# Optimization experiments

Hardware: AMD Instinct MI355X
Metric: run time of the kernel (lower is better)

The kernel has to match this reference:

```python
import jax, jax.numpy as jnp
import numpy as np

STRIDE = 1
PAD = 1


def setup_inputs() -> dict:
    key = jax.random.key(0)
    k1, k2, k3 = jax.random.split(key, 3)
    # Single image (C_in, H, W) as in the original unbatched HETensor list layout
    x = jax.random.normal(k1, (256, 512, 512), dtype=jnp.float32)
    # Weights in HWIO layout (kh, kw, C_in, C_out) matching load_weights' expected shape
    W = jax.random.normal(k2, (3, 3, 256, 256), dtype=jnp.float32) * 0.02
    b = jax.random.normal(k3, (256,), dtype=jnp.float32)
    return {"x": x, "W": W, "b": b}


def reference(x, W, b):
    # Zero-pad then convolve; out_h = ceil((H + 2*PAD - kh + 1)/STRIDE) == lax conv output for stride 1
    out = jax.lax.conv_general_dilated(
        x[None],                      # [1, C_in, H, W]
        W,                            # [kh, kw, C_in, C_out]
        window_strides=(STRIDE, STRIDE),
        padding=[(PAD, PAD), (PAD, PAD)],
        dimension_numbers=("NCHW", "HWIO", "NCHW"),
    )
    return out[0] + b[:, None, None]  # [C_out, H, W]
```

## Files before the change

kernel.cpp:

```cpp
#include <hip/hip_runtime.h>
#include <hip/hip_bf16.h>


typedef __attribute__((ext_vector_type(8))) short bf16x8;
typedef __attribute__((ext_vector_type(4))) float floatx4;

#define HWSZ 262144
#define CIN  256
#define HH   512
#define WWD  512

__device__ __forceinline__ void async_copy16(const void* g, void* l) {
  __builtin_amdgcn_global_load_lds(
      (const __attribute__((address_space(1))) void*)g,
      (__attribute__((address_space(3))) void*)l, 16, 0, 0);
}

__global__ __launch_bounds__(256) void convert_x(
    const float* __restrict__ x, __hip_bfloat16* __restrict__ xt)
{
  __shared__ __align__(16) unsigned char lds[64 * 512];
  const int b  = blockIdx.x;
  const int wt = b & 7;
  const int h  = b >> 3;
  const int w0 = wt << 6;
  const int t  = threadIdx.x;

  const int lane16 = t & 15;
  const int cidx   = t >> 4;
  const float* xrow = x + (size_t)h * WWD + w0 + lane16 * 4;
#pragma unroll 4
  for (int cit = 0; cit < 16; ++cit) {
    int ci = cit * 16 + cidx;
    float4 v = *(const float4*)(xrow + (size_t)ci * HWSZ);
    float f[4] = {v.x, v.y, v.z, v.w};
#pragma unroll
    for (int j = 0; j < 4; ++j) {
      int p = lane16 * 4 + j;
      int chunk = (ci >> 3) ^ (p >> 2);
      *(__hip_bfloat16*)&lds[p * 512 + chunk * 16 + (ci & 7) * 2] =
          __float2bfloat16(f[j]);
    }
  }
  __syncthreads();

  const int m  = t & 31;
  const int pq = t >> 5;
#pragma unroll
  for (int it = 0; it < 8; ++it) {
    int p = it * 8 + pq;
    uint4 v = *(const uint4*)&lds[p * 512 + ((m ^ (p >> 2)) << 4)];
    *(uint4*)&xt[(((size_t)h * WWD + w0 + p) << 8) + m * 8] = v;
  }
}

__global__ __launch_bounds__(256) void convert_w(
    const float* __restrict__ Wf, __hip_bfloat16* __restrict__ wt,
    __hip_bfloat16* __restrict__ zb)
{
  const int idx = blockIdx.x * 256 + threadIdx.x;
  const int ci = idx & 255;
  const int co = (idx >> 8) & 255;
  const int kk = idx >> 16;
  wt[((size_t)(kk * 256 + co) << 8) + ci] =
      __float2bfloat16(Wf[((size_t)(kk * 256 + ci) << 8) + co]);
  if (idx < 64) zb[idx] = __float2bfloat16(0.0f);
}

__global__ __launch_bounds__(256, 3) void conv_mfma(
    const __hip_bfloat16* __restrict__ xt,
    const __hip_bfloat16* __restrict__ wt,
    const float* __restrict__ bias,
    float* __restrict__ out,
    const __hip_bfloat16* __restrict__ zb)
{
  __shared__ __align__(16) __hip_bfloat16 As[3 * 128 * 32];
  __shared__ __align__(16) __hip_bfloat16 Bs[130 * 32];

  const int b    = blockIdx.x;
  const int wti  = b & 3;
  const int cot  = (b >> 2) & 1;
  const int h    = b >> 3;
  const int w0   = wti << 7;
  const int co0  = cot << 7;
  const int t    = threadIdx.x;
  const int lane = t & 63;
  const int wave = t >> 6;
  const int wm   = wave & 1;
  const int wn   = wave >> 1;
  const int mcol = lane & 15;
  const int krow = lane >> 4;

  floatx4 acc[4][4];
#pragma unroll
  for (int mi = 0; mi < 4; ++mi)
#pragma unroll
    for (int ni = 0; ni < 4; ++ni) {
      floatx4 z = {0.f, 0.f, 0.f, 0.f};
      acc[mi][ni] = z;
    }

  for (int kh = 0; kh < 3; ++kh) {
    const int hp = h + kh - 1;
    const bool hok = (unsigned)hp < (unsigned)HH;
    const __hip_bfloat16* xrow = xt + (size_t)hp * (WWD * CIN);

    for (int ci0 = 0; ci0 < CIN; ci0 += 32) {
      __syncthreads();
#pragma unroll
      for (int rnd = 0; rnd < 6; ++rnd) {
        int c  = rnd * 256 + t;
        int kw = c >> 9;
        int m  = (c >> 2) & 127;
        int j  = c & 3;
        const __hip_bfloat16* g =
            wt + (((size_t)((kh * 3 + kw) * 256 + co0 + m)) << 8) + ci0 + (j << 3);
        async_copy16(g, &As[c << 3]);
      }
#pragma unroll
      for (int rnd = 0; rnd < 2; ++rnd) {
        int c = rnd * 256 + t;
        int r = c >> 2;
        int j = c & 3;
        int wp = w0 - 1 + r;
        const __hip_bfloat16* g = (hok && (unsigned)wp < (unsigned)WWD)
            ? xrow + ((size_t)wp << 8) + ci0 + (j << 3)
            : zb + (j << 3);
        async_copy16(g, &Bs[c << 3]);
      }
      if (t < 8) {
        int c = 512 + t;
        int r = c >> 2;
        int j = c & 3;
        int wp = w0 - 1 + r;
        const __hip_bfloat16* g = (hok && (unsigned)wp < (unsigned)WWD)
            ? xrow + ((size_t)wp << 8) + ci0 + (j << 3)
            : zb + (j << 3);
        async_copy16(g, &Bs[c << 3]);
      }
      __syncthreads();

#pragma unroll
      for (int kw = 0; kw < 3; ++kw) {
        bf16x8 af[4], bfr[4];
#pragma unroll
        for (int mi = 0; mi < 4; ++mi)
          af[mi] = *(const bf16x8*)&As[(kw << 12) + ((wm * 64 + mi * 16 + mcol) << 5) + (krow << 3)];
#pragma unroll
        for (int ni = 0; ni < 4; ++ni)
          bfr[ni] = *(const bf16x8*)&Bs[((wn * 64 + ni * 16 + mcol + kw) << 5) + (krow << 3)];
#pragma unroll
        for (int mi = 0; mi < 4; ++mi)
#pragma unroll
          for (int ni = 0; ni < 4; ++ni)
            acc[mi][ni] = __builtin_amdgcn_mfma_f32_16x16x32_bf16(
                af[mi], bfr[ni], acc[mi][ni], 0, 0, 0);
      }
    }
  }

  const size_t outrow = (size_t)h * WWD;
#pragma unroll
  for (int mi = 0; mi < 4; ++mi) {
#pragma unroll
    for (int r = 0; r < 4; ++r) {
      int co = co0 + wm * 64 + mi * 16 + krow * 4 + r;
      float bv = bias[co];
      float* op = out + (size_t)co * HWSZ + outrow + w0 + wn * 64 + mcol;
#pragma unroll
      for (int ni = 0; ni < 4; ++ni)
        op[ni * 16] = acc[mi][ni][r] + bv;
    }
  }
}

__global__ __launch_bounds__(256) void conv_naive(
    const float* __restrict__ x, const float* __restrict__ Wf,
    const float* __restrict__ bias, float* __restrict__ out)
{
  size_t idx = (size_t)blockIdx.x * 256 + threadIdx.x;
  int w  = (int)(idx & 511);
  int h  = (int)((idx >> 9) & 511);
  int co = (int)(idx >> 18);
  float acc = bias[co];
  for (int kh = 0; kh < 3; ++kh) {
    int hp = h + kh - 1;
    if ((unsigned)hp >= 512u) continue;
    for (int kw = 0; kw < 3; ++kw) {
      int wp = w + kw - 1;
      if ((unsigned)wp >= 512u) continue;
      const float* wcol = Wf + ((size_t)(kh * 3 + kw) << 16) + co;
      const float* xpix = x + (size_t)hp * 512 + wp;
      for (int ci = 0; ci < 256; ++ci)
        acc += xpix[(size_t)ci * HWSZ] * wcol[(size_t)ci << 8];
    }
  }
  out[idx] = acc;
}

extern "C" void kernel_launch(void* const* d_in, const int* in_sizes, int n_in,
                              void* d_out, int out_size, void* d_ws, size_t ws_size,
                              hipStream_t stream) {
  const float* x    = (const float*)d_in[0];
  const float* Wf   = (const float*)d_in[1];
  const float* bias = (const float*)d_in[2];
  float* out = (float*)d_out;

  const size_t xt_bytes = (size_t)HH * WWD * CIN * 2;
  const size_t wt_bytes = (size_t)9 * 256 * 256 * 2;
  const size_t need = xt_bytes + wt_bytes + 256;

  if (ws_size >= need) {
    __hip_bfloat16* xt = (__hip_bfloat16*)d_ws;
    __hip_bfloat16* wt = (__hip_bfloat16*)((char*)d_ws + xt_bytes);
    __hip_bfloat16* zb = (__hip_bfloat16*)((char*)d_ws + xt_bytes + wt_bytes);
    convert_x<<<4096, 256, 0, stream>>>(x, xt);
    convert_w<<<2304, 256, 0, stream>>>(Wf, wt, zb);
    conv_mfma<<<4096, 256, 0, stream>>>(xt, wt, bias, out, zb);
  } else {
    conv_naive<<<262144, 256, 0, stream>>>(x, Wf, bias, out);
  }
}
```

Measured before the change: 709.2 us.

## Widen convert_x tiles with packed LDS writes and remap conv blocks per XCD

The input transpose kernel now handles 128 pixels with 512 threads. It loads four channels per thread so it can write packed 8-byte bf16 groups into LDS with a new swizzle, replacing single 2-byte stores. The conv kernel remaps block indices so that consecutive rows h are assigned to the same XCD (blockIdx mod 8). The aim is better L2 reuse of the overlapping input rows across the 3 kh taps. The larger convert_x tile uses more LDS, which may limit occupancy.

```diff
diff --git a/kernel.cpp b/kernel.cpp
--- a/kernel.cpp
+++ b/kernel.cpp
@@ -16,30 +16,41 @@
       (__attribute__((address_space(3))) void*)l, 16, 0, 0);
 }
 
-__global__ __launch_bounds__(256) void convert_x(
+__global__ __launch_bounds__(512, 4) void convert_x(
     const float* __restrict__ x, __hip_bfloat16* __restrict__ xt)
 {
-  __shared__ __align__(16) unsigned char lds[64 * 512];
+  __shared__ __align__(16) unsigned char lds[128 * 512];
   const int b  = blockIdx.x;
-  const int wt = b & 7;
-  const int h  = b >> 3;
-  const int w0 = wt << 6;
+  const int wt = b & 3;
+  const int h  = b >> 2;
+  const int w0 = wt << 7;
   const int t  = threadIdx.x;
 
-  const int lane16 = t & 15;
-  const int cidx   = t >> 4;
-  const float* xrow = x + (size_t)h * WWD + w0 + lane16 * 4;
-#pragma unroll 4
-  for (int cit = 0; cit < 16; ++cit) {
-    int ci = cit * 16 + cidx;
-    float4 v = *(const float4*)(xrow + (size_t)ci * HWSZ);
-    float f[4] = {v.x, v.y, v.z, v.w};
+  const int wq  = t & 31;
+  const int cg  = t >> 5;
+  const int swz = (wq & 15) << 1;
+  const float* xbase = x + (size_t)h * WWD + w0 + wq * 4;
+#pragma unroll
+  for (int it = 0; it < 4; ++it) {
+    int s  = it * 16 + cg;
+    int ci = s << 2;
+    float4 v0 = *(const float4*)(xbase + (size_t)(ci + 0) * HWSZ);
+    float4 v1 = *(const float4*)(xbase + (size_t)(ci + 1) * HWSZ);
+    float4 v2 = *(const float4*)(xbase + (size_t)(ci + 2) * HWSZ);
+    float4 v3 = *(const float4*)(xbase + (size_t)(ci + 3) * HWSZ);
 #pragma unroll
     for (int j = 0; j < 4; ++j) {
-      int p = lane16 * 4 + j;
-      int chunk = (ci >> 3) ^ (p >> 2);
-      *(__hip_bfloat16*)&lds[p * 512 + chunk * 16 + (ci & 7) * 2] =
-          __float2bfloat16(f[j]);
+      int p = (wq << 2) + j;
+      __hip_bfloat16 b0 = __float2bfloat16(((const float*)&v0)[j]);
+      __hip_bfloat16 b1 = __float2bfloat16(((const float*)&v1)[j]);
+      __hip_bfloat16 b2 = __float2bfloat16(((const float*)&v2)[j]);
+      __hip_bfloat16 b3 = __float2bfloat16(((const float*)&v3)[j]);
+      ushort4 u;
+      u.x = *(const unsigned short*)&b0;
+      u.y = *(const unsigned short*)&b1;
+      u.z = *(const unsigned short*)&b2;
+      u.w = *(const unsigned short*)&b3;
+      *(ushort4*)&lds[p * 512 + ((s ^ swz) << 3)] = u;
     }
   }
   __syncthreads();
@@ -48,8 +59,8 @@
   const int pq = t >> 5;
 #pragma unroll
   for (int it = 0; it < 8; ++it) {
-    int p = it * 8 + pq;
-    uint4 v = *(const uint4*)&lds[p * 512 + ((m ^ (p >> 2)) << 4)];
+    int p = it * 16 + pq;
+    uint4 v = *(const uint4*)&lds[p * 512 + ((m ^ ((p >> 2) & 15)) << 4)];
     *(uint4*)&xt[(((size_t)h * WWD + w0 + p) << 8) + m * 8] = v;
   }
 }
@@ -77,10 +88,13 @@
   __shared__ __align__(16) __hip_bfloat16 As[3 * 128 * 32];
   __shared__ __align__(16) __hip_bfloat16 Bs[130 * 32];
 
-  const int b    = blockIdx.x;
-  const int wti  = b & 3;
-  const int cot  = (b >> 2) & 1;
-  const int h    = b >> 3;
+  const int b     = blockIdx.x;
+  const int xcd   = b & 7;
+  const int local = b >> 3;
+  const int h     = (xcd << 6) + (local >> 3);
+  const int rem   = local & 7;
+  const int cot   = rem >> 2;
+  const int wti   = rem & 3;
   const int w0   = wti << 7;
   const int co0  = cot << 7;
   const int t    = threadIdx.x;
@@ -214,7 +228,7 @@
     __hip_bfloat16* xt = (__hip_bfloat16*)d_ws;
     __hip_bfloat16* wt = (__hip_bfloat16*)((char*)d_ws + xt_bytes);
     __hip_bfloat16* zb = (__hip_bfloat16*)((char*)d_ws + xt_bytes + wt_bytes);
-    convert_x<<<4096, 256, 0, stream>>>(x, xt);
+    convert_x<<<2048, 512, 0, stream>>>(x, xt);
     convert_w<<<2304, 256, 0, stream>>>(Wf, wt, zb);
     conv_mfma<<<4096, 256, 0, stream>>>(xt, wt, bias, out, zb);
   } else {
```

Measured after the change: 706.3 us. No clear change (-0.4%).

## Switch bf16 staging to channel-group-blocked layout and remap blocks per XCD

Applied to the files above, without the earlier changes.

The intermediate bf16 activation and weight buffers move from channel-last to a layout blocked by groups of 8 channels, [h][cg][w][8] and [kk][cg][co][8]. Async LDS loads then read contiguous 16-byte chunks across neighbouring pixels or output channels. convert_x is rewritten without LDS: each thread converts one pixel's 8 channels per step with strided scalar loads, and the launch uses 1024 blocks. The conv kernel remaps block indices so each XCD handles a contiguous band of rows for L2 locality of shared input rows, and raises launch-bounds occupancy from 3 to 4, which risks register spills.

```diff
diff --git a/kernel.cpp b/kernel.cpp
--- a/kernel.cpp
+++ b/kernel.cpp
@@ -19,38 +19,26 @@
 __global__ __launch_bounds__(256) void convert_x(
     const float* __restrict__ x, __hip_bfloat16* __restrict__ xt)
 {
-  __shared__ __align__(16) unsigned char lds[64 * 512];
-  const int b  = blockIdx.x;
-  const int wt = b & 7;
-  const int h  = b >> 3;
-  const int w0 = wt << 6;
-  const int t  = threadIdx.x;
-
-  const int lane16 = t & 15;
-  const int cidx   = t >> 4;
-  const float* xrow = x + (size_t)h * WWD + w0 + lane16 * 4;
-#pragma unroll 4
-  for (int cit = 0; cit < 16; ++cit) {
-    int ci = cit * 16 + cidx;
-    float4 v = *(const float4*)(xrow + (size_t)ci * HWSZ);
-    float f[4] = {v.x, v.y, v.z, v.w};
-#pragma unroll
-    for (int j = 0; j < 4; ++j) {
-      int p = lane16 * 4 + j;
-      int chunk = (ci >> 3) ^ (p >> 2);
-      *(__hip_bfloat16*)&lds[p * 512 + chunk * 16 + (ci & 7) * 2] =
-          __float2bfloat16(f[j]);
-    }
-  }
-  __syncthreads();
-
-  const int m  = t & 31;
-  const int pq = t >> 5;
-#pragma unroll
-  for (int it = 0; it < 8; ++it) {
-    int p = it * 8 + pq;
-    uint4 v = *(const uint4*)&lds[p * 512 + ((m ^ (p >> 2)) << 4)];
-    *(uint4*)&xt[(((size_t)h * WWD + w0 + p) << 8) + m * 8] = v;
+  const int b = blockIdx.x;
+  const int h = b >> 1;
+  const int w = ((b & 1) << 8) + threadIdx.x;
+  const float* xp = x + (size_t)h * WWD + w;
+#pragma unroll 2
+  for (int cg = 0; cg < 32; ++cg) {
+    const float* s = xp + (size_t)(cg << 3) * HWSZ;
+    unsigned int q[4];
+#pragma unroll
+    for (int k = 0; k < 4; ++k) {
+      float f0 = s[(size_t)(2 * k) * HWSZ];
+      float f1 = s[(size_t)(2 * k + 1) * HWSZ];
+      __hip_bfloat16 b0 = __float2bfloat16(f0);
+      __hip_bfloat16 b1 = __float2bfloat16(f1);
+      q[k] = (unsigned int)*(const unsigned short*)&b0 |
+             ((unsigned int)*(const unsigned short*)&b1 << 16);
+    }
+    uint4 v;
+    v.x = q[0]; v.y = q[1]; v.z = q[2]; v.w = q[3];
+    *(uint4*)&xt[(((size_t)h * 32 + cg) << 12) + ((size_t)w << 3)] = v;
   }
 }
 
@@ -62,12 +50,12 @@
   const int ci = idx & 255;
   const int co = (idx >> 8) & 255;
   const int kk = idx >> 16;
-  wt[((size_t)(kk * 256 + co) << 8) + ci] =
+  wt[(((size_t)(kk * 32 + (ci >> 3)) * 256 + co) << 3) + (ci & 7)] =
       __float2bfloat16(Wf[((size_t)(kk * 256 + ci) << 8) + co]);
   if (idx < 64) zb[idx] = __float2bfloat16(0.0f);
 }
 
-__global__ __launch_bounds__(256, 3) void conv_mfma(
+__global__ __launch_bounds__(256, 4) void conv_mfma(
     const __hip_bfloat16* __restrict__ xt,
     const __hip_bfloat16* __restrict__ wt,
     const float* __restrict__ bias,
@@ -77,10 +65,13 @@
   __shared__ __align__(16) __hip_bfloat16 As[3 * 128 * 32];
   __shared__ __align__(16) __hip_bfloat16 Bs[130 * 32];
 
-  const int b    = blockIdx.x;
-  const int wti  = b & 3;
-  const int cot  = (b >> 2) & 1;
-  const int h    = b >> 3;
+  const int b     = blockIdx.x;
+  const int xcd   = b & 7;
+  const int local = b >> 3;
+  const int h     = (xcd << 6) + (local >> 3);
+  const int rem   = local & 7;
+  const int cot   = rem >> 2;
+  const int wti   = rem & 3;
   const int w0   = wti << 7;
   const int co0  = cot << 7;
   const int t    = threadIdx.x;
@@ -103,9 +94,10 @@
   for (int kh = 0; kh < 3; ++kh) {
     const int hp = h + kh - 1;
     const bool hok = (unsigned)hp < (unsigned)HH;
-    const __hip_bfloat16* xrow = xt + (size_t)hp * (WWD * CIN);
+    const __hip_bfloat16* xrow = xt + ((size_t)hp << 17);
 
     for (int ci0 = 0; ci0 < CIN; ci0 += 32) {
+      const int cg0 = ci0 >> 3;
       __syncthreads();
 #pragma unroll
       for (int rnd = 0; rnd < 6; ++rnd) {
@@ -114,7 +106,7 @@
         int m  = (c >> 2) & 127;
         int j  = c & 3;
         const __hip_bfloat16* g =
-            wt + (((size_t)((kh * 3 + kw) * 256 + co0 + m)) << 8) + ci0 + (j << 3);
+            wt + (((size_t)((kh * 3 + kw) * 32 + cg0 + j)) << 11) + ((co0 + m) << 3);
         async_copy16(g, &As[c << 3]);
       }
 #pragma unroll
@@ -124,7 +116,7 @@
         int j = c & 3;
         int wp = w0 - 1 + r;
         const __hip_bfloat16* g = (hok && (unsigned)wp < (unsigned)WWD)
-            ? xrow + ((size_t)wp << 8) + ci0 + (j << 3)
+            ? xrow + ((size_t)(cg0 + j) << 12) + (wp << 3)
             : zb + (j << 3);
         async_copy16(g, &Bs[c << 3]);
       }
@@ -134,7 +126,7 @@
         int j = c & 3;
         int wp = w0 - 1 + r;
         const __hip_bfloat16* g = (hok && (unsigned)wp < (unsigned)WWD)
-            ? xrow + ((size_t)wp << 8) + ci0 + (j << 3)
+            ? xrow + ((size_t)(cg0 + j) << 12) + (wp << 3)
             : zb + (j << 3);
         async_copy16(g, &Bs[c << 3]);
       }
@@ -214,7 +206,7 @@
     __hip_bfloat16* xt = (__hip_bfloat16*)d_ws;
     __hip_bfloat16* wt = (__hip_bfloat16*)((char*)d_ws + xt_bytes);
     __hip_bfloat16* zb = (__hip_bfloat16*)((char*)d_ws + xt_bytes + wt_bytes);
-    convert_x<<<4096, 256, 0, stream>>>(x, xt);
+    convert_x<<<1024, 256, 0, stream>>>(x, xt);
     convert_w<<<2304, 256, 0, stream>>>(Wf, wt, zb);
     conv_mfma<<<4096, 256, 0, stream>>>(xt, wt, bias, out, zb);
   } else {
```

After: 1.007 ms. 1.42x slower.
